# Performance work log

Measured on AMD Instinct MI355X. Metric: run time of the kernel, lower is better.

## Reference

```python
import jax, jax.numpy as jnp
import numpy as np

N = 100000
NNZ = 3200000
K = 3

def setup_inputs() -> dict:
    key = jax.random.key(0)
    ks = jax.random.split(key, 9)
    return {
        "x": jax.random.normal(ks[0], (N, 128), dtype=jnp.float32),
        "vals": jax.random.uniform(ks[1], (NNZ,), dtype=jnp.float32) * (1.0 / 32.0),
        "W1": jax.random.normal(ks[2], (128 * K, 256), dtype=jnp.float32) * 0.05,
        "b1": jax.random.normal(ks[3], (256,), dtype=jnp.float32) * 0.05,
        "W2": jax.random.normal(ks[4], (256 * K, 64), dtype=jnp.float32) * 0.05,
        "b2": jax.random.normal(ks[5], (64,), dtype=jnp.float32) * 0.05,
        "rows": jax.random.randint(ks[6], (NNZ,), 0, N, dtype=jnp.int32),
        "cols": jax.random.randint(ks[7], (NNZ,), 0, N, dtype=jnp.int32),
        "idx": jax.random.randint(ks[8], (50000,), 0, N, dtype=jnp.int32),
    }

def _spmm(rows, cols, vals, x):
    # sparse [N,N] @ dense [N,F] via gather + segment_sum
    return jax.ops.segment_sum(vals[:, None] * x[cols], rows, num_segments=N)

def _cheb_basis(x, rows, cols, vals, k):
    # Chebyshev recurrence: T0=x, T1=L x, T_m = 2 L T_{m-1} - T_{m-2}
    xs = [x]
    if k > 1:
        x0, x1 = x, _spmm(rows, cols, vals, x)
        xs.append(x1)
        for _ in range(2, k):
            x2 = 2.0 * _spmm(rows, cols, vals, x1) - x0
            xs.append(x2)
            x0, x1 = x1, x2
    # match torch layout: [N, F, K] -> [N, F*K] (per-feature K contiguous)
    return jnp.stack(xs, axis=2).reshape(x.shape[0], -1)

def reference(x, vals, W1, b1, W2, b2, rows, cols, idx):
    h = _cheb_basis(x, rows, cols, vals, K) @ W1 + b1
    h = jax.nn.relu(h)  # dropout omitted (eval mode)
    out = _cheb_basis(h, rows, cols, vals, K) @ W2 + b2
    return out[idx]
```

## Files before the change

kernel.cpp:

```cpp
#include <hip/hip_runtime.h>
#include <hip/hip_bf16.h>

typedef __attribute__((ext_vector_type(8))) __bf16 bf16x8;
typedef __attribute__((ext_vector_type(4))) float floatx4;
typedef unsigned short ushort_t;
typedef unsigned int uint_t;

#define N_NODES 100000
#define NNZ_E   3200000
#define N_IDX   50000
#define NB_BKT  196
#define PTILE   8192
#define PBLOCKS 391

__device__ __forceinline__ float bf2f(uint_t u16) {
  union { float f; uint_t i; } v; v.i = u16 << 16; return v.f;
}
__device__ __forceinline__ unsigned short f2bf(float f) {
  union { float f; uint_t i; } v; v.f = f;
  uint_t x = v.i;
  return (unsigned short)((x + 0x7FFFu + ((x >> 16) & 1u)) >> 16);
}


__global__ __launch_bounds__(256) void k_bhist(const int* __restrict__ rows,
                                               int* __restrict__ bcnt) {
  __shared__ int h[NB_BKT];
  for (int i = threadIdx.x; i < NB_BKT; i += 256) h[i] = 0;
  __syncthreads();
  int base = blockIdx.x * PTILE;
  for (int i = threadIdx.x; i < PTILE; i += 256) {
    int e = base + i;
    if (e < NNZ_E) atomicAdd(&h[rows[e] >> 9], 1);
  }
  __syncthreads();
  for (int i = threadIdx.x; i < NB_BKT; i += 256)
    if (h[i]) atomicAdd(&bcnt[i], h[i]);
}

__global__ void k_bscan(const int* __restrict__ bcnt, int* __restrict__ bbase,
                        int* __restrict__ bcur) {
  __shared__ int ts[256];
  int t = threadIdx.x;
  int v = (t < NB_BKT) ? bcnt[t] : 0;
  ts[t] = v;
  __syncthreads();
  for (int off = 1; off < 256; off <<= 1) {
    int x = ts[t];
    int a = (t >= off) ? ts[t - off] : 0;
    __syncthreads();
    ts[t] = x + a;
    __syncthreads();
  }
  if (t < NB_BKT) {
    int b = (t == 0) ? 0 : ts[t - 1];
    bbase[t] = b;
    bcur[t] = b;
  }
}

__global__ __launch_bounds__(256) void k_part(const int* __restrict__ rows,
                                              const int* __restrict__ cols,
                                              const float* __restrict__ vals,
                                              int* __restrict__ bcur,
                                              int2* __restrict__ tmp) {
  __shared__ int h[NB_BKT];
  for (int i = threadIdx.x; i < NB_BKT; i += 256) h[i] = 0;
  __syncthreads();
  int base = blockIdx.x * PTILE;
  for (int i = threadIdx.x; i < PTILE; i += 256) {
    int e = base + i;
    if (e < NNZ_E) atomicAdd(&h[rows[e] >> 9], 1);
  }
  __syncthreads();
  for (int i = threadIdx.x; i < NB_BKT; i += 256) {
    int c = h[i];
    h[i] = c ? atomicAdd(&bcur[i], c) : 0;
  }
  __syncthreads();
  for (int i = threadIdx.x; i < PTILE; i += 256) {
    int e = base + i;
    if (e < NNZ_E) {
      int rr = rows[e];
      int p = atomicAdd(&h[rr >> 9], 1);
      int2 o;
      o.x = cols[e] | ((rr & 511) << 17);
      o.y = __float_as_int(vals[e]);
      tmp[p] = o;
    }
  }
}

__global__ __launch_bounds__(512) void k_sort(const int* __restrict__ bbase,
                                              const int2* __restrict__ tmp,
                                              int2* __restrict__ edges,
                                              int* __restrict__ rowptr) {
  __shared__ int cnt[512];
  __shared__ int ts[512];
  int b = blockIdx.x, t = threadIdx.x;
  int s = bbase[b];
  int epos = (b == NB_BKT - 1) ? NNZ_E : bbase[b + 1];
  cnt[t] = 0;
  __syncthreads();
  for (int i = s + t; i < epos; i += 512)
    atomicAdd(&cnt[(tmp[i].x >> 17) & 511], 1);
  __syncthreads();
  ts[t] = cnt[t];
  __syncthreads();
  for (int off = 1; off < 512; off <<= 1) {
    int x = ts[t];
    int a = (t >= off) ? ts[t - off] : 0;
    __syncthreads();
    ts[t] = x + a;
    __syncthreads();
  }
  int pre = (t == 0) ? 0 : ts[t - 1];
  int grow = b * 512 + t;
  if (grow < N_NODES) rowptr[grow] = s + pre;
  cnt[t] = s + pre;
  __syncthreads();
  for (int i = s + t; i < epos; i += 512) {
    int2 p = tmp[i];
    int rl = (p.x >> 17) & 511;
    int pos = atomicAdd(&cnt[rl], 1);
    int2 o;
    o.x = (p.x & 0x1FFFF) << 8;
    o.y = p.y;
    edges[pos] = o;
  }
  if (b == 0 && t == 0) rowptr[N_NODES] = NNZ_E;
}


__global__ void k_cvt(const float4* __restrict__ x, ushort4* __restrict__ xb) {
  int i = blockIdx.x * blockDim.x + threadIdx.x;
  if (i < N_NODES * 128 / 4) {
    float4 v = x[i];
    ushort4 o;
    o.x = f2bf(v.x); o.y = f2bf(v.y); o.z = f2bf(v.z); o.w = f2bf(v.w);
    xb[i] = o;
  }
}


__global__ void k_prepW1(const float* __restrict__ W, ushort_t* __restrict__ Wp) {
  int kp = blockIdx.x;
  int n  = threadIdx.x;
  int ch = kp >> 7;
  int f  = kp & 127;
  float v;
  if (ch == 0)      v = W[(f*3+0)*256+n] - W[(f*3+2)*256+n];
  else if (ch == 1) v = W[(f*3+1)*256+n];
  else              v = 2.0f * W[(f*3+2)*256+n];
  int kb = kp >> 5, kr = kp & 31;
  int lane = ((kr >> 3) << 4) | (n & 15);
  Wp[(((size_t)kb * 16 + (n >> 4)) * 64 + lane) * 8 + (kr & 7)] = f2bf(v);
}

__global__ void k_prepW2(const float* __restrict__ W, ushort_t* __restrict__ Wp) {
  int f = blockIdx.x;
  int c = threadIdx.x;
  int g = c >> 6, n = c & 63;
  float v;
  if (g == 0)      v = W[(f*3+0)*64+n] - W[(f*3+2)*64+n];
  else if (g == 1) v = W[(f*3+1)*64+n];
  else             v = 2.0f * W[(f*3+2)*64+n];
  int kb = f >> 5, kr = f & 31;
  int nb = c >> 4;
  int lane = ((kr >> 3) << 4) | (c & 15);
  Wp[(((size_t)kb * 12 + nb) * 64 + lane) * 8 + (kr & 7)] = f2bf(v);
}


__global__ __launch_bounds__(256) void k_spmm128(
    const int* __restrict__ rowptr, const int2* __restrict__ edges,
    const ushort_t* __restrict__ in, ushort_t* __restrict__ out) {
  int r = blockIdx.x * 4 + (threadIdx.x >> 6);
  int f = threadIdx.x & 63;
  uint_t fo = (uint_t)f << 2;
  const char* inb = (const char*)in;
  int e0 = rowptr[r], e1 = rowptr[r + 1];
  float a0 = 0.f, a1 = 0.f;
  int e = e0;
  for (; e + 16 <= e1; e += 16) {
    int2 E[16];
#pragma unroll
    for (int j = 0; j < 16; ++j) E[j] = edges[e + j];
    uint_t q[16];
#pragma unroll
    for (int j = 0; j < 16; ++j)
      q[j] = *(const uint_t*)(inb + (((uint_t)E[j].x) | fo));
#pragma unroll
    for (int j = 0; j < 16; ++j) {
      float v = __int_as_float(E[j].y);
      a0 = fmaf(v, bf2f(q[j] & 0xFFFFu), a0);
      a1 = fmaf(v, bf2f(q[j] >> 16), a1);
    }
  }
  for (; e + 4 <= e1; e += 4) {
    int2 E[4];
#pragma unroll
    for (int j = 0; j < 4; ++j) E[j] = edges[e + j];
#pragma unroll
    for (int j = 0; j < 4; ++j) {
      uint_t q = *(const uint_t*)(inb + (((uint_t)E[j].x) | fo));
      float v = __int_as_float(E[j].y);
      a0 = fmaf(v, bf2f(q & 0xFFFFu), a0);
      a1 = fmaf(v, bf2f(q >> 16), a1);
    }
  }
  for (; e < e1; ++e) {
    int2 E = edges[e];
    uint_t q = *(const uint_t*)(inb + (((uint_t)E.x) | fo));
    float v = __int_as_float(E.y);
    a0 = fmaf(v, bf2f(q & 0xFFFFu), a0);
    a1 = fmaf(v, bf2f(q >> 16), a1);
  }
  uint_t o = ((uint_t)f2bf(a1) << 16) | (uint_t)f2bf(a0);
  *(uint_t*)(out + (size_t)r * 128 + 2 * f) = o;
}


__global__ __launch_bounds__(256) void k_spmm64_add(
    const int* __restrict__ rowptr, const int2* __restrict__ edges,
    const ushort_t* __restrict__ p2, const ushort_t* __restrict__ p1,
    ushort_t* __restrict__ u) {
  int r = blockIdx.x * 4 + (threadIdx.x >> 6);
  int lane = threadIdx.x & 63;
  int half = lane >> 5, f = lane & 31;
  uint_t fo = (uint_t)f << 2;
  const char* pb = (const char*)p2;
  int e0 = rowptr[r], e1 = rowptr[r + 1];
  int ne = e1 - e0;
  int hs = (ne + 1) >> 1;
  int e = e0 + half * hs;
  int send = half ? e1 : (e0 + hs);
  float a0 = 0.f, a1 = 0.f;
  for (; e + 8 <= send; e += 8) {
    int2 E[8];
#pragma unroll
    for (int j = 0; j < 8; ++j) E[j] = edges[e + j];
    uint_t q[8];
#pragma unroll
    for (int j = 0; j < 8; ++j)
      q[j] = *(const uint_t*)(pb + ((((uint_t)E[j].x) >> 1) | fo));
#pragma unroll
    for (int j = 0; j < 8; ++j) {
      float v = __int_as_float(E[j].y);
      a0 = fmaf(v, bf2f(q[j] & 0xFFFFu), a0);
      a1 = fmaf(v, bf2f(q[j] >> 16), a1);
    }
  }
  for (; e < send; ++e) {
    int2 E = edges[e];
    uint_t q = *(const uint_t*)(pb + ((((uint_t)E.x) >> 1) | fo));
    float v = __int_as_float(E.y);
    a0 = fmaf(v, bf2f(q & 0xFFFFu), a0);
    a1 = fmaf(v, bf2f(q >> 16), a1);
  }
  a0 += __shfl_xor(a0, 32);
  a1 += __shfl_xor(a1, 32);
  if (half == 0) {
    uint_t pp = *(const uint_t*)(p1 + (size_t)r * 64 + 2 * f);
    float b0 = a0 + bf2f(pp & 0xFFFFu);
    float b1 = a1 + bf2f(pp >> 16);
    uint_t o = ((uint_t)f2bf(b1) << 16) | (uint_t)f2bf(b0);
    *(uint_t*)(u + (size_t)r * 64 + 2 * f) = o;
  }
}


__global__ __launch_bounds__(256) void k_spmm64_idx(
    const int* __restrict__ rowptr, const int2* __restrict__ edges,
    const ushort_t* __restrict__ u, const float* __restrict__ p0,
    const int* __restrict__ idx, float* __restrict__ out) {
  int o = blockIdx.x * 4 + (threadIdx.x >> 6);
  int r = idx[o];
  int lane = threadIdx.x & 63;
  int half = lane >> 5, f = lane & 31;
  uint_t fo = (uint_t)f << 2;
  const char* ub = (const char*)u;
  int e0 = rowptr[r], e1 = rowptr[r + 1];
  int ne = e1 - e0;
  int hs = (ne + 1) >> 1;
  int e = e0 + half * hs;
  int send = half ? e1 : (e0 + hs);
  float a0 = 0.f, a1 = 0.f;
  for (; e + 8 <= send; e += 8) {
    int2 E[8];
#pragma unroll
    for (int j = 0; j < 8; ++j) E[j] = edges[e + j];
    uint_t q[8];
#pragma unroll
    for (int j = 0; j < 8; ++j)
      q[j] = *(const uint_t*)(ub + ((((uint_t)E[j].x) >> 1) | fo));
#pragma unroll
    for (int j = 0; j < 8; ++j) {
      float v = __int_as_float(E[j].y);
      a0 = fmaf(v, bf2f(q[j] & 0xFFFFu), a0);
      a1 = fmaf(v, bf2f(q[j] >> 16), a1);
    }
  }
  for (; e < send; ++e) {
    int2 E = edges[e];
    uint_t q = *(const uint_t*)(ub + ((((uint_t)E.x) >> 1) | fo));
    float v = __int_as_float(E.y);
    a0 = fmaf(v, bf2f(q & 0xFFFFu), a0);
    a1 = fmaf(v, bf2f(q >> 16), a1);
  }
  a0 += __shfl_xor(a0, 32);
  a1 += __shfl_xor(a1, 32);
  if (half == 0) {
    float2 b = *(const float2*)(p0 + (size_t)r * 64 + 2 * f);
    float2 w; w.x = b.x + a0; w.y = b.y + a1;
    *(float2*)(out + (size_t)o * 64 + 2 * f) = w;
  }
}


__global__ __launch_bounds__(256) void k_gemm1(
    const ushort_t* __restrict__ A0, const ushort_t* __restrict__ A1,
    const ushort_t* __restrict__ A2, const ushort_t* __restrict__ Bp,
    const float* __restrict__ bias, ushort_t* __restrict__ h) {
  int wid = (blockIdx.x * 256 + threadIdx.x) >> 6;
  int lane = threadIdx.x & 63;
  int mt = wid >> 1, ng = wid & 1;
  int mr = mt * 16 + (lane & 15);
  int ko = (lane >> 4) << 3;
  floatx4 acc[8] = {};
#pragma unroll
  for (int c = 0; c < 3; ++c) {
    const ushort_t* Ab = (c == 0 ? A0 : c == 1 ? A1 : A2) + (size_t)mr * 128 + ko;
#pragma unroll
    for (int kb = 0; kb < 4; ++kb) {
      bf16x8 a = *(const bf16x8*)(Ab + kb * 32);
      int kbg = c * 4 + kb;
      const ushort_t* Bb = Bp + (((size_t)(kbg * 16 + ng * 8)) * 64 + lane) * 8;
#pragma unroll
      for (int nt = 0; nt < 8; ++nt) {
        bf16x8 b = *(const bf16x8*)(Bb + (size_t)nt * 64 * 8);
        acc[nt] = __builtin_amdgcn_mfma_f32_16x16x32_bf16(a, b, acc[nt], 0, 0, 0);
      }
    }
  }
  int col0 = ng * 128 + (lane & 15);
  int r0 = mt * 16 + ((lane >> 4) << 2);
#pragma unroll
  for (int nt = 0; nt < 8; ++nt) {
    int col = col0 + nt * 16;
    float bv = bias[col];
#pragma unroll
    for (int rg = 0; rg < 4; ++rg) {
      float v = acc[nt][rg] + bv;
      v = v > 0.f ? v : 0.f;
      h[(size_t)(r0 + rg) * 256 + col] = f2bf(v);
    }
  }
}


__global__ __launch_bounds__(256) void k_gemm2(
    const ushort_t* __restrict__ A, const ushort_t* __restrict__ Bp,
    const float* __restrict__ bias, float* __restrict__ p0,
    ushort_t* __restrict__ p1, ushort_t* __restrict__ p2) {
  int wid = (blockIdx.x * 256 + threadIdx.x) >> 6;
  if (wid >= 18750) return;
  int lane = threadIdx.x & 63;
  int mt = wid / 3, ng = wid - mt * 3;
  int mr = mt * 16 + (lane & 15);
  int ko = (lane >> 4) << 3;
  floatx4 acc[4] = {};
  const ushort_t* Ab = A + (size_t)mr * 256 + ko;
#pragma unroll
  for (int kb = 0; kb < 8; ++kb) {
    bf16x8 a = *(const bf16x8*)(Ab + kb * 32);
    const ushort_t* Bb = Bp + (((size_t)(kb * 12 + ng * 4)) * 64 + lane) * 8;
#pragma unroll
    for (int nt = 0; nt < 4; ++nt) {
      bf16x8 b = *(const bf16x8*)(Bb + (size_t)nt * 64 * 8);
      acc[nt] = __builtin_amdgcn_mfma_f32_16x16x32_bf16(a, b, acc[nt], 0, 0, 0);
    }
  }
  int c16 = lane & 15;
  int r0 = mt * 16 + ((lane >> 4) << 2);
  if (ng == 0) {
#pragma unroll
    for (int nt = 0; nt < 4; ++nt) {
      float bv = bias[nt * 16 + c16];
#pragma unroll
      for (int rg = 0; rg < 4; ++rg)
        p0[(size_t)(r0 + rg) * 64 + nt * 16 + c16] = acc[nt][rg] + bv;
    }
  } else {
    ushort_t* dst = (ng == 1) ? p1 : p2;
#pragma unroll
    for (int nt = 0; nt < 4; ++nt)
#pragma unroll
      for (int rg = 0; rg < 4; ++rg)
        dst[(size_t)(r0 + rg) * 64 + nt * 16 + c16] = f2bf(acc[nt][rg]);
  }
}


extern "C" void kernel_launch(void* const* d_in, const int* in_sizes, int n_in,
                              void* d_out, int out_size, void* d_ws, size_t ws_size,
                              hipStream_t stream) {
  const float* x    = (const float*)d_in[0];
  const float* vals = (const float*)d_in[1];
  const float* W1   = (const float*)d_in[2];
  const float* b1   = (const float*)d_in[3];
  const float* W2   = (const float*)d_in[4];
  const float* b2   = (const float*)d_in[5];
  const int*   rows = (const int*)d_in[6];
  const int*   cols = (const int*)d_in[7];
  const int*   idx  = (const int*)d_in[8];
  float* out = (float*)d_out;

  char* w = (char*)d_ws;
  size_t off = 0;
  auto take = [&](size_t b) -> char* {
    char* p = w + off;
    off += (b + 255) & ~(size_t)255;
    return p;
  };
  int*      bcnt    = (int*)take((size_t)NB_BKT * 4);
  int*      bbase   = (int*)take((size_t)NB_BKT * 4);
  int*      bcur    = (int*)take((size_t)NB_BKT * 4);
  int*      rowptr  = (int*)take((size_t)(N_NODES + 1) * 4);
  int2*     tmp     = (int2*)take((size_t)NNZ_E * 8);
  int2*     edges   = (int2*)take((size_t)NNZ_E * 8);
  ushort_t* xb      = (ushort_t*)take((size_t)N_NODES * 128 * 2);
  ushort_t* T1a     = (ushort_t*)take((size_t)N_NODES * 128 * 2);
  ushort_t* U1      = (ushort_t*)take((size_t)N_NODES * 128 * 2);
  ushort_t* h       = (ushort_t*)take((size_t)N_NODES * 256 * 2);
  ushort_t* W1p     = (ushort_t*)take((size_t)384 * 256 * 2);
  ushort_t* W2p     = (ushort_t*)take((size_t)256 * 192 * 2);

  float*    p0 = (float*)xb;
  ushort_t* p1 = T1a;
  ushort_t* p2 = T1a + (size_t)N_NODES * 64;
  ushort_t* u  = U1;

  hipMemsetAsync(bcnt, 0, (size_t)NB_BKT * 4, stream);
  k_bhist<<<PBLOCKS, 256, 0, stream>>>(rows, bcnt);
  k_bscan<<<1, 256, 0, stream>>>(bcnt, bbase, bcur);
  k_part<<<PBLOCKS, 256, 0, stream>>>(rows, cols, vals, bcur, tmp);
  k_sort<<<NB_BKT, 512, 0, stream>>>(bbase, tmp, edges, rowptr);

  k_cvt<<<(N_NODES * 128 / 4 + 255) / 256, 256, 0, stream>>>((const float4*)x, (ushort4*)xb);
  k_prepW1<<<384, 256, 0, stream>>>(W1, W1p);
  k_prepW2<<<256, 192, 0, stream>>>(W2, W2p);

  k_spmm128<<<N_NODES / 4, 256, 0, stream>>>(rowptr, edges, xb, T1a);
  k_spmm128<<<N_NODES / 4, 256, 0, stream>>>(rowptr, edges, T1a, U1);
  k_gemm1<<<3125, 256, 0, stream>>>(xb, T1a, U1, W1p, b1, h);

  k_gemm2<<<4688, 256, 0, stream>>>(h, W2p, b2, p0, p1, p2);
  k_spmm64_add<<<N_NODES / 4, 256, 0, stream>>>(rowptr, edges, p2, p1, u);
  k_spmm64_idx<<<N_IDX / 4, 256, 0, stream>>>(rowptr, edges, u, p0, idx, out);
}
```

Before: 691.8 us.

## Use finer row buckets for edge sort and compute all gemm2 outputs per wave

The bucket size for the two-pass CSR construction drops from 512 rows to 128, giving 782 buckets instead of 196. This gives the local sort kernel many more, smaller blocks of 256 threads to spread over the GPU's compute units, and the bucket scan grows to 1024 threads. Separately, gemm2 now has each wave compute all 12 N-tiles for a 16-row strip, instead of splitting the three output groups across three waves. That loads each A fragment once rather than three times, at the cost of more accumulator registers per wave and fewer waves overall.

```diff
diff --git a/kernel.cpp b/kernel.cpp
--- a/kernel.cpp
+++ b/kernel.cpp
@@ -9,7 +9,8 @@
 #define N_NODES 100000
 #define NNZ_E   3200000
 #define N_IDX   50000
-#define NB_BKT  196
+#define NB_BKT  782
+#define ROWS_PB 128
 #define PTILE   8192
 #define PBLOCKS 391
 
@@ -31,21 +32,22 @@
   int base = blockIdx.x * PTILE;
   for (int i = threadIdx.x; i < PTILE; i += 256) {
     int e = base + i;
-    if (e < NNZ_E) atomicAdd(&h[rows[e] >> 9], 1);
+    if (e < NNZ_E) atomicAdd(&h[rows[e] >> 7], 1);
   }
   __syncthreads();
   for (int i = threadIdx.x; i < NB_BKT; i += 256)
     if (h[i]) atomicAdd(&bcnt[i], h[i]);
 }
 
-__global__ void k_bscan(const int* __restrict__ bcnt, int* __restrict__ bbase,
-                        int* __restrict__ bcur) {
-  __shared__ int ts[256];
+__global__ __launch_bounds__(1024) void k_bscan(const int* __restrict__ bcnt,
+                                                int* __restrict__ bbase,
+                                                int* __restrict__ bcur) {
+  __shared__ int ts[1024];
   int t = threadIdx.x;
   int v = (t < NB_BKT) ? bcnt[t] : 0;
   ts[t] = v;
   __syncthreads();
-  for (int off = 1; off < 256; off <<= 1) {
+  for (int off = 1; off < 1024; off <<= 1) {
     int x = ts[t];
     int a = (t >= off) ? ts[t - off] : 0;
     __syncthreads();
@@ -70,7 +72,7 @@
   int base = blockIdx.x * PTILE;
   for (int i = threadIdx.x; i < PTILE; i += 256) {
     int e = base + i;
-    if (e < NNZ_E) atomicAdd(&h[rows[e] >> 9], 1);
+    if (e < NNZ_E) atomicAdd(&h[rows[e] >> 7], 1);
   }
   __syncthreads();
   for (int i = threadIdx.x; i < NB_BKT; i += 256) {
@@ -82,46 +84,48 @@
     int e = base + i;
     if (e < NNZ_E) {
       int rr = rows[e];
-      int p = atomicAdd(&h[rr >> 9], 1);
+      int p = atomicAdd(&h[rr >> 7], 1);
       int2 o;
-      o.x = cols[e] | ((rr & 511) << 17);
+      o.x = cols[e] | ((rr & 127) << 17);
       o.y = __float_as_int(vals[e]);
       tmp[p] = o;
     }
   }
 }
 
-__global__ __launch_bounds__(512) void k_sort(const int* __restrict__ bbase,
+__global__ __launch_bounds__(256) void k_sort(const int* __restrict__ bbase,
                                               const int2* __restrict__ tmp,
                                               int2* __restrict__ edges,
                                               int* __restrict__ rowptr) {
-  __shared__ int cnt[512];
-  __shared__ int ts[512];
+  __shared__ int cnt[ROWS_PB];
+  __shared__ int ts[ROWS_PB];
   int b = blockIdx.x, t = threadIdx.x;
   int s = bbase[b];
   int epos = (b == NB_BKT - 1) ? NNZ_E : bbase[b + 1];
-  cnt[t] = 0;
-  __syncthreads();
-  for (int i = s + t; i < epos; i += 512)
-    atomicAdd(&cnt[(tmp[i].x >> 17) & 511], 1);
-  __syncthreads();
-  ts[t] = cnt[t];
-  __syncthreads();
-  for (int off = 1; off < 512; off <<= 1) {
-    int x = ts[t];
-    int a = (t >= off) ? ts[t - off] : 0;
+  if (t < ROWS_PB) cnt[t] = 0;
+  __syncthreads();
+  for (int i = s + t; i < epos; i += 256)
+    atomicAdd(&cnt[(tmp[i].x >> 17) & 127], 1);
+  __syncthreads();
+  if (t < ROWS_PB) ts[t] = cnt[t];
+  __syncthreads();
+  for (int off = 1; off < ROWS_PB; off <<= 1) {
+    int x = 0, a = 0;
+    if (t < ROWS_PB) { x = ts[t]; a = (t >= off) ? ts[t - off] : 0; }
     __syncthreads();
-    ts[t] = x + a;
+    if (t < ROWS_PB) ts[t] = x + a;
     __syncthreads();
   }
-  int pre = (t == 0) ? 0 : ts[t - 1];
-  int grow = b * 512 + t;
-  if (grow < N_NODES) rowptr[grow] = s + pre;
-  cnt[t] = s + pre;
-  __syncthreads();
-  for (int i = s + t; i < epos; i += 512) {
+  if (t < ROWS_PB) {
+    int pre = (t == 0) ? 0 : ts[t - 1];
+    int grow = b * ROWS_PB + t;
+    if (grow < N_NODES) rowptr[grow] = s + pre;
+    cnt[t] = s + pre;
+  }
+  __syncthreads();
+  for (int i = s + t; i < epos; i += 256) {
     int2 p = tmp[i];
-    int rl = (p.x >> 17) & 511;
+    int rl = (p.x >> 17) & 127;
     int pos = atomicAdd(&cnt[rl], 1);
     int2 o;
     o.x = (p.x & 0x1FFFF) << 8;
@@ -364,41 +368,41 @@
     const float* __restrict__ bias, float* __restrict__ p0,
     ushort_t* __restrict__ p1, ushort_t* __restrict__ p2) {
   int wid = (blockIdx.x * 256 + threadIdx.x) >> 6;
-  if (wid >= 18750) return;
+  if (wid >= 6250) return;
   int lane = threadIdx.x & 63;
-  int mt = wid / 3, ng = wid - mt * 3;
-  int mr = mt * 16 + (lane & 15);
+  int mr = wid * 16 + (lane & 15);
   int ko = (lane >> 4) << 3;
-  floatx4 acc[4] = {};
+  floatx4 acc[12] = {};
   const ushort_t* Ab = A + (size_t)mr * 256 + ko;
 #pragma unroll
   for (int kb = 0; kb < 8; ++kb) {
     bf16x8 a = *(const bf16x8*)(Ab + kb * 32);
-    const ushort_t* Bb = Bp + (((size_t)(kb * 12 + ng * 4)) * 64 + lane) * 8;
-#pragma unroll
-    for (int nt = 0; nt < 4; ++nt) {
+    const ushort_t* Bb = Bp + (((size_t)kb * 12) * 64 + lane) * 8;
+#pragma unroll
+    for (int nt = 0; nt < 12; ++nt) {
       bf16x8 b = *(const bf16x8*)(Bb + (size_t)nt * 64 * 8);
       acc[nt] = __builtin_amdgcn_mfma_f32_16x16x32_bf16(a, b, acc[nt], 0, 0, 0);
     }
   }
   int c16 = lane & 15;
-  int r0 = mt * 16 + ((lane >> 4) << 2);
-  if (ng == 0) {
-#pragma unroll
-    for (int nt = 0; nt < 4; ++nt) {
-      float bv = bias[nt * 16 + c16];
-#pragma unroll
-      for (int rg = 0; rg < 4; ++rg)
-        p0[(size_t)(r0 + rg) * 64 + nt * 16 + c16] = acc[nt][rg] + bv;
-    }
-  } else {
-    ushort_t* dst = (ng == 1) ? p1 : p2;
-#pragma unroll
-    for (int nt = 0; nt < 4; ++nt)
-#pragma unroll
-      for (int rg = 0; rg < 4; ++rg)
-        dst[(size_t)(r0 + rg) * 64 + nt * 16 + c16] = f2bf(acc[nt][rg]);
-  }
+  int r0 = wid * 16 + ((lane >> 4) << 2);
+#pragma unroll
+  for (int nt = 0; nt < 4; ++nt) {
+    float bv = bias[nt * 16 + c16];
+#pragma unroll
+    for (int rg = 0; rg < 4; ++rg)
+      p0[(size_t)(r0 + rg) * 64 + nt * 16 + c16] = acc[nt][rg] + bv;
+  }
+#pragma unroll
+  for (int nt = 4; nt < 8; ++nt)
+#pragma unroll
+    for (int rg = 0; rg < 4; ++rg)
+      p1[(size_t)(r0 + rg) * 64 + (nt - 4) * 16 + c16] = f2bf(acc[nt][rg]);
+#pragma unroll
+  for (int nt = 8; nt < 12; ++nt)
+#pragma unroll
+    for (int rg = 0; rg < 4; ++rg)
+      p2[(size_t)(r0 + rg) * 64 + (nt - 8) * 16 + c16] = f2bf(acc[nt][rg]);
 }
 
 
@@ -443,9 +447,9 @@
 
   hipMemsetAsync(bcnt, 0, (size_t)NB_BKT * 4, stream);
   k_bhist<<<PBLOCKS, 256, 0, stream>>>(rows, bcnt);
-  k_bscan<<<1, 256, 0, stream>>>(bcnt, bbase, bcur);
+  k_bscan<<<1, 1024, 0, stream>>>(bcnt, bbase, bcur);
   k_part<<<PBLOCKS, 256, 0, stream>>>(rows, cols, vals, bcur, tmp);
-  k_sort<<<NB_BKT, 512, 0, stream>>>(bbase, tmp, edges, rowptr);
+  k_sort<<<NB_BKT, 256, 0, stream>>>(bbase, tmp, edges, rowptr);
 
   k_cvt<<<(N_NODES * 128 / 4 + 255) / 256, 256, 0, stream>>>((const float4*)x, (ushort4*)xb);
   k_prepW1<<<384, 256, 0, stream>>>(W1, W1p);
@@ -455,7 +459,7 @@
   k_spmm128<<<N_NODES / 4, 256, 0, stream>>>(rowptr, edges, T1a, U1);
   k_gemm1<<<3125, 256, 0, stream>>>(xb, T1a, U1, W1p, b1, h);
 
-  k_gemm2<<<4688, 256, 0, stream>>>(h, W2p, b2, p0, p1, p2);
+  k_gemm2<<<1563, 256, 0, stream>>>(h, W2p, b2, p0, p1, p2);
   k_spmm64_add<<<N_NODES / 4, 256, 0, stream>>>(rowptr, edges, p2, p1, u);
   k_spmm64_idx<<<N_IDX / 4, 256, 0, stream>>>(rowptr, edges, u, p0, idx, out);
 }
```

Result: no change. 699.4 us (+1.1%).
